# Performance work log

Measured on AMD Instinct MI355X. Metric: run time of the kernel, lower is better.

Reference implementation:

```python
import math
import jax, jax.numpy as jnp
import numpy as np

N = 256  # size (power of 2)
B = 512  # batch
STEEPNESS = 10.0  # cauchy distribution steepness


def _bitonic_network(n):
    # n must be a power of 2; every layer then has exactly n//2 compare-exchanges.
    num_blocks = int(math.log2(n))
    sa_l, sb_l, cmin_l, cmax_l = [], [], [], []
    for block_idx in range(num_blocks):
        for layer_idx in range(block_idx + 1):
            m = 2 ** (block_idx - layer_idx)
            split_a = np.zeros((n // 2, n), np.float32)
            split_b = np.zeros((n // 2, n), np.float32)
            combine_min = np.zeros((n, n // 2), np.float32)
            combine_max = np.zeros((n, n // 2), np.float32)
            count = 0
            for i in range(0, n, 2 * m):
                for j in range(m):
                    ix = i + j
                    a, b = ix, ix + m
                    split_a[count, a] = 1.0
                    split_b[count, b] = 1.0
                    if (ix // 2 ** (block_idx + 1)) % 2 == 1:
                        a, b = b, a
                    combine_min[a, count] = 1.0
                    combine_max[b, count] = 1.0
                    count += 1
            sa_l.append(split_a); sb_l.append(split_b)
            cmin_l.append(combine_min); cmax_l.append(combine_max)
    return (np.stack(sa_l), np.stack(sb_l), np.stack(cmin_l), np.stack(cmax_l))


def setup_inputs() -> dict:
    key = jax.random.key(0)
    vectors = jax.random.normal(key, (B, N), dtype=jnp.float32)
    sa, sb, cmin, cmax = _bitonic_network(N)
    return {
        "vectors": vectors,
        "split_a": jnp.asarray(sa),       # [L, n/2, n]
        "split_b": jnp.asarray(sb),       # [L, n/2, n]
        "combine_min": jnp.asarray(cmin), # [L, n, n/2]
        "combine_max": jnp.asarray(cmax), # [L, n, n/2]
    }


def reference(vectors, split_a, split_b, combine_min, combine_max):
    # Faithful to the given source: x (=vectors) is never updated inside the
    # loop; only the soft permutation matrix X is accumulated and returned.
    Bsz, n = vectors.shape
    X0 = jnp.broadcast_to(jnp.eye(n, dtype=vectors.dtype), (Bsz, n, n))

    def step(X, mats):
        sa, sb, cmin, cmax = mats
        a = vectors @ sa.T  # [B, k]
        b = vectors @ sb.T  # [B, k]
        # cauchy interpolation
        alpha = jnp.arctan(STEEPNESS * (b - a)) / jnp.pi + 0.5  # [B, k]
        aX = jnp.einsum('bij,kj->bik', X, sa)  # [B, n, k]
        bX = jnp.einsum('bij,kj->bik', X, sb)  # [B, n, k]
        al = alpha[:, None, :]
        w_min = al * aX + (1.0 - al) * bX
        w_max = (1.0 - al) * aX + al * bX
        X_new = jnp.einsum('bik,jk->bij', w_max, cmax) + jnp.einsum('bik,jk->bij', w_min, cmin)
        return X_new, None

    X, _ = jax.lax.scan(step, X0, (split_a, split_b, combine_min, combine_max))
    return X
```

## Files before the change

### kernel.cpp

```cpp
#include <hip/hip_runtime.h>
#include <math.h>

typedef float vf4 __attribute__((ext_vector_type(4)));

static constexpr int LLB[36] = {
  0,
  1,0,
  2,1,0,
  3,2,1,0,
  4,3,2,1,0,
  5,4,3,2,1,0,
  6,5,4,3,2,1,0,
  7,6,5,4,3,2,1,0
};
static constexpr int LBLK[36] = {
  0,
  1,1,
  2,2,2,
  3,3,3,3,
  4,4,4,4,4,
  5,5,5,5,5,5,
  6,6,6,6,6,6,6,
  7,7,7,7,7,7,7,7
};

#define BF(ARR, KL, UU) { \
  const int p_ = (((KL) >> lb) << (lb + 1)) | ((KL) & (m - 1)); \
  const int q_ = p_ + m; \
  const float t_  = ARR[p_] - ARR[q_]; \
  const float np_ = fmaf((UU), t_, ARR[q_]); \
  const float nq_ = fmaf(-(UU), t_, ARR[p_]); \
  ARR[p_] = np_; ARR[q_] = nq_; }

__global__ __launch_bounds__(256) void k_gen1(const float* __restrict__ vec,
                                              float* __restrict__ U2,
                                              float4* __restrict__ staged2) {
  const int b = blockIdx.x;
  const int tid = threadIdx.x;
  __shared__ __align__(16) float ub[36 * 128];
  __shared__ float vv[256];
  vv[tid] = vec[b * 256 + tid];
  __syncthreads();

  const int k = tid & 127;
  if (tid < 128) {
    #pragma unroll
    for (int l = 0; l < 18; ++l) {
      const int lb = LLB[l], blk = LBLK[l];
      const int m = 1 << lb;
      const int p = ((k >> lb) << (lb + 1)) | (k & (m - 1));
      const int q = p + m;
      const int d = (p >> (blk + 1)) & 1;
      const float alpha =
          atanf(10.0f * (vv[q] - vv[p])) * 0.3183098861837907f + 0.5f;
      ub[l * 128 + k] = d ? (1.0f - alpha) : alpha;
    }
  } else {
    #pragma unroll
    for (int l = 18; l < 36; ++l) {
      const int lb = LLB[l], blk = LBLK[l];
      const int m = 1 << lb;
      const int p = ((k >> lb) << (lb + 1)) | (k & (m - 1));
      const int q = p + m;
      const int d = (p >> (blk + 1)) & 1;
      const float alpha =
          atanf(10.0f * (vv[q] - vv[p])) * 0.3183098861837907f + 0.5f;
      const float u = d ? (1.0f - alpha) : alpha;
      ub[l * 128 + k] = u;
      if (l >= 21) U2[b * 1920 + (l - 21) * 128 + k] = u;
    }
  }
  __syncthreads();

  const int g  = tid >> 6;
  const int il = tid & 63;
  float r[64];
  #pragma unroll
  for (int j = 0; j < 64; ++j) r[j] = (j == il) ? 1.0f : 0.0f;

  #pragma unroll
  for (int l = 0; l < 21; ++l) {
    const int lb = LLB[l];
    const int m = 1 << lb;
    const float4* ulv = (const float4*)(ub + l * 128 + 32 * g);
    #pragma unroll
    for (int t = 0; t < 8; ++t) {
      const float4 u4 = ulv[t];
      BF(r, 4*t+0, u4.x)
      BF(r, 4*t+1, u4.y)
      BF(r, 4*t+2, u4.z)
      BF(r, 4*t+3, u4.w)
    }
  }

  float4* sp = staged2 + ((size_t)(b * 4 + g) * 16) * 64 + il;
  #pragma unroll
  for (int t = 0; t < 16; ++t)
    sp[t * 64] = make_float4(r[4*t], r[4*t+1], r[4*t+2], r[4*t+3]);
}

__global__ __launch_bounds__(256) void k_phase23(const float* __restrict__ U2,
                                                 const float4* __restrict__ staged2,
                                                 float* __restrict__ out) {
  const int bg = blockIdx.x;
  const int b = bg >> 2;
  const int g = bg & 3;
  const int c  = threadIdx.x >> 6;
  const int rr = threadIdx.x & 63;
  __shared__ float4 ex[2048];
  float y[64];

  const int ub2 = __builtin_amdgcn_readfirstlane(b * 1920);
  const int ap = g >> 1;
  const bool part = ((c >> 1) == ap);
  const int cb = __builtin_amdgcn_readfirstlane(32 * c);

  if (part) {
    const bool sm = ((c & 1) == (g & 1));
    const float* u21 = U2 + ub2 + 64 * ap;
    const float4* sp = staged2 + ((size_t)(b * 4 + g) * 16) * 64 + rr;
    #pragma unroll
    for (int t = 0; t < 16; ++t) {
      const float4 s4 = sp[t * 64];
      const float u0 = u21[4*t+0], u1 = u21[4*t+1];
      const float u2 = u21[4*t+2], u3 = u21[4*t+3];
      y[4*t+0] = s4.x * (sm ? u0 : 1.0f - u0);
      y[4*t+1] = s4.y * (sm ? u1 : 1.0f - u1);
      y[4*t+2] = s4.z * (sm ? u2 : 1.0f - u2);
      y[4*t+3] = s4.w * (sm ? u3 : 1.0f - u3);
    }
    #pragma unroll
    for (int l = 22; l < 28; ++l) {
      const int lb = LLB[l];
      const int m = 1 << lb;
      const float* ul = U2 + ub2 + (l - 21) * 128 + cb;
      #pragma unroll
      for (int kl = 0; kl < 32; ++kl) {
        const float u = ul[kl];
        BF(y, kl, u)
      }
    }
  }

  {
    const float* u28 = U2 + ub2 + 7 * 128 + 64 * (c & 1);
    if (part) {
      #pragma unroll
      for (int t = 0; t < 16; ++t)
        ex[((c & 1) * 16 + t) * 64 + rr] =
            make_float4(y[4*t], y[4*t+1], y[4*t+2], y[4*t+3]);
    }
    __syncthreads();
    if (part) {
      #pragma unroll
      for (int t = 0; t < 16; ++t) {
        y[4*t+0] *= u28[4*t+0];
        y[4*t+1] *= u28[4*t+1];
        y[4*t+2] *= u28[4*t+2];
        y[4*t+3] *= u28[4*t+3];
      }
    } else {
      #pragma unroll
      for (int t = 0; t < 16; ++t) {
        const float4 p4 = ex[((c & 1) * 16 + t) * 64 + rr];
        y[4*t+0] = fmaf(-u28[4*t+0], p4.x, p4.x);
        y[4*t+1] = fmaf(-u28[4*t+1], p4.y, p4.y);
        y[4*t+2] = fmaf(-u28[4*t+2], p4.z, p4.z);
        y[4*t+3] = fmaf(-u28[4*t+3], p4.w, p4.w);
      }
    }
    __syncthreads();
  }

  {
    const float* u29 = U2 + ub2 + 8 * 128 + 64 * (c >> 1);
    const int pc = c ^ 1;
    #pragma unroll
    for (int t = 0; t < 8; ++t)
      ex[(c * 8 + t) * 64 + rr] =
          make_float4(y[4*t], y[4*t+1], y[4*t+2], y[4*t+3]);
    __syncthreads();
    #pragma unroll
    for (int t = 0; t < 8; ++t) {
      const float4 p4 = ex[(pc * 8 + t) * 64 + rr];
      y[4*t+0] = fmaf(u29[4*t+0], y[4*t+0] - p4.x, p4.x);
      y[4*t+1] = fmaf(u29[4*t+1], y[4*t+1] - p4.y, p4.y);
      y[4*t+2] = fmaf(u29[4*t+2], y[4*t+2] - p4.z, p4.z);
      y[4*t+3] = fmaf(u29[4*t+3], y[4*t+3] - p4.w, p4.w);
    }
    __syncthreads();
    #pragma unroll
    for (int t = 8; t < 16; ++t)
      ex[(c * 8 + (t - 8)) * 64 + rr] =
          make_float4(y[4*t], y[4*t+1], y[4*t+2], y[4*t+3]);
    __syncthreads();
    #pragma unroll
    for (int t = 8; t < 16; ++t) {
      const float4 p4 = ex[(pc * 8 + (t - 8)) * 64 + rr];
      y[4*t+0] = fmaf(u29[4*t+0], y[4*t+0] - p4.x, p4.x);
      y[4*t+1] = fmaf(u29[4*t+1], y[4*t+1] - p4.y, p4.y);
      y[4*t+2] = fmaf(u29[4*t+2], y[4*t+2] - p4.z, p4.z);
      y[4*t+3] = fmaf(u29[4*t+3], y[4*t+3] - p4.w, p4.w);
    }
    __syncthreads();
  }

  #pragma unroll
  for (int l = 30; l < 36; ++l) {
    const int lb = LLB[l];
    const int m = 1 << lb;
    const float* ul = U2 + ub2 + (l - 21) * 128 + cb;
    #pragma unroll
    for (int kl = 0; kl < 32; ++kl) {
      const float u = ul[kl];
      BF(y, kl, u)
    }
  }

  float4* out4 = (float4*)out + ((size_t)(b * 256 + g * 64)) * 64;
  const int tid = threadIdx.x;

  if (rr < 32) {
    #pragma unroll
    for (int t = 0; t < 16; ++t)
      ex[rr * 64 + ((c * 16 + t) ^ (rr & 7))] =
          make_float4(y[4*t], y[4*t+1], y[4*t+2], y[4*t+3]);
  }
  __syncthreads();
  #pragma unroll
  for (int it = 0; it < 8; ++it) {
    const int fq = it * 256 + tid;
    const int r_ = fq >> 6;
    const int q_ = fq & 63;
    const float4 v4 = ex[r_ * 64 + (q_ ^ (r_ & 7))];
    __builtin_nontemporal_store(*(const vf4*)&v4, (vf4*)&out4[fq]);
  }
  __syncthreads();
  if (rr >= 32) {
    #pragma unroll
    for (int t = 0; t < 16; ++t)
      ex[(rr - 32) * 64 + ((c * 16 + t) ^ (rr & 7))] =
          make_float4(y[4*t], y[4*t+1], y[4*t+2], y[4*t+3]);
  }
  __syncthreads();
  #pragma unroll
  for (int it = 0; it < 8; ++it) {
    const int fq = it * 256 + tid;
    const int r_ = fq >> 6;
    const int q_ = fq & 63;
    const float4 v4 = ex[r_ * 64 + (q_ ^ (r_ & 7))];
    __builtin_nontemporal_store(*(const vf4*)&v4, (vf4*)&out4[2048 + fq]);
  }
}

extern "C" void kernel_launch(void* const* d_in, const int* in_sizes, int n_in,
                              void* d_out, int out_size, void* d_ws, size_t ws_size,
                              hipStream_t stream) {
  const float* vec = (const float*)d_in[0];
  float* out = (float*)d_out;
  float* U2 = (float*)d_ws;
  float4* staged2 = (float4*)(U2 + (size_t)512 * 1920);

  hipLaunchKernelGGL(k_gen1,    dim3(512),  dim3(256), 0, stream, vec, U2, staged2);
  hipLaunchKernelGGL(k_phase23, dim3(2048), dim3(256), 0, stream, U2, staged2, out);
}
```

Measured before the change: 186.4 us.

## Split rows across lane quads with DPP butterflies and LDS-cached weights

Rewrites the second-phase kernel so each row of the permutation matrix is spread across four lanes. The smallest-stride compare-exchange layers now use DPP lane swaps instead of LDS exchange rounds with block barriers. The per-batch interpolation weights are staged once in shared memory, and the first kernel writes them in a permuted order so that float4 reads line up with the new lane mapping. This is meant to cut LDS round-trips, barriers and global weight loads, at the cost of more complex indexing and a strict dependence on the staging layout matching between the two kernels.

Result: slower. 193.9 us (+4.0%).

```diff
diff --git a/kernel.cpp b/kernel.cpp
--- a/kernel.cpp
+++ b/kernel.cpp
@@ -24,14 +24,6 @@
   7,7,7,7,7,7,7,7
 };
 
-#define BF(ARR, KL, UU) { \
-  const int p_ = (((KL) >> lb) << (lb + 1)) | ((KL) & (m - 1)); \
-  const int q_ = p_ + m; \
-  const float t_  = ARR[p_] - ARR[q_]; \
-  const float np_ = fmaf((UU), t_, ARR[q_]); \
-  const float nq_ = fmaf(-(UU), t_, ARR[p_]); \
-  ARR[p_] = np_; ARR[q_] = nq_; }
-
 __global__ __launch_bounds__(256) void k_gen1(const float* __restrict__ vec,
                                               float* __restrict__ U2,
                                               float4* __restrict__ staged2) {
@@ -66,8 +58,13 @@
       const float alpha =
           atanf(10.0f * (vv[q] - vv[p])) * 0.3183098861837907f + 0.5f;
       const float u = d ? (1.0f - alpha) : alpha;
-      ub[l * 128 + k] = u;
-      if (l >= 21) U2[b * 1920 + (l - 21) * 128 + k] = u;
+      if (l < 21) ub[l * 128 + k] = u;
+      if (l >= 21) {
+        int pos;
+        if (lb >= 2) pos = (k >> 4) * 16 + (k & 3) * 4 + ((k >> 2) & 3);
+        else         pos = (k >> 3) * 8  + (k & 1) * 4 + ((k >> 1) & 3);
+        U2[b * 1920 + (l - 21) * 128 + pos] = u;
+      }
     }
   }
   __syncthreads();
@@ -86,10 +83,18 @@
     #pragma unroll
     for (int t = 0; t < 8; ++t) {
       const float4 u4 = ulv[t];
-      BF(r, 4*t+0, u4.x)
-      BF(r, 4*t+1, u4.y)
-      BF(r, 4*t+2, u4.z)
-      BF(r, 4*t+3, u4.w)
+      #pragma unroll
+      for (int c = 0; c < 4; ++c) {
+        const int kl = 4 * t + c;
+        const int p = ((kl >> lb) << (lb + 1)) | (kl & (m - 1));
+        const int q = p + m;
+        const float u = (c == 0) ? u4.x : (c == 1) ? u4.y : (c == 2) ? u4.z : u4.w;
+        const float t_  = r[p] - r[q];
+        const float np = fmaf(u, t_, r[q]);
+        const float nq = fmaf(-u, t_, r[p]);
+        r[p] = np;
+        r[q] = nq;
+      }
     }
   }
 
@@ -99,157 +104,128 @@
     sp[t * 64] = make_float4(r[4*t], r[4*t+1], r[4*t+2], r[4*t+3]);
 }
 
-__global__ __launch_bounds__(256) void k_phase23(const float* __restrict__ U2,
-                                                 const float4* __restrict__ staged2,
-                                                 float* __restrict__ out) {
+
+#define BFP(KK, LBP, UU) { \
+  const int mp_ = 1 << (LBP); \
+  const int p_ = (((KK) >> (LBP)) << ((LBP) + 1)) | ((KK) & (mp_ - 1)); \
+  const float t_ = y[p_] - y[p_ + mp_]; \
+  const float np_ = fmaf((UU), t_, y[p_ + mp_]); \
+  const float nq_ = fmaf(-(UU), t_, y[p_]); \
+  y[p_] = np_; y[p_ + mp_] = nq_; }
+
+#define INL(LI, LBP, K0, NP) { \
+  const float4* uL4 = (const float4*)(up + (LI) * 128) + t4; \
+  _Pragma("unroll") \
+  for (int kg = (K0) >> 2; kg < ((K0) + (NP)) >> 2; ++kg) { \
+    const float4 u4 = uL4[kg * 4]; \
+    BFP(4*kg+0, LBP, u4.x) BFP(4*kg+1, LBP, u4.y) \
+    BFP(4*kg+2, LBP, u4.z) BFP(4*kg+3, LBP, u4.w) } }
+
+#define DPPBF(AA, XM, UU) { \
+  const float pv_ = __int_as_float(__builtin_amdgcn_mov_dpp( \
+      __float_as_int(y[AA]), (XM), 0xF, 0xF, false)); \
+  y[AA] = fmaf((UU), y[AA] - pv_, pv_); }
+
+#define DPPL(LI, XM, SEL, A0, NA) { \
+  const float4* uD4 = (const float4*)(up + (LI) * 128) + (SEL); \
+  _Pragma("unroll") \
+  for (int ag = (A0) >> 2; ag < ((A0) + (NA)) >> 2; ++ag) { \
+    const float4 u4 = uD4[ag * 2]; \
+    DPPBF(4*ag+0, XM, u4.x) DPPBF(4*ag+1, XM, u4.y) \
+    DPPBF(4*ag+2, XM, u4.z) DPPBF(4*ag+3, XM, u4.w) } }
+
+#define LOADY(BASE) { \
+  _Pragma("unroll") \
+  for (int j = 0; j < 16; ++j) y[(BASE) + j] = sp[j * 256]; }
+
+#define BLK6(RB) { \
+  INL(0, 4, (RB)/2, 16)   \
+  INL(1, 3, (RB)/2, 16)   \
+  INL(2, 2, (RB)/2, 16)   \
+  INL(3, 1, (RB)/2, 16)   \
+  INL(4, 0, (RB)/2, 16)   \
+  DPPL(5, 0x4E, (t4 & 1),  (RB), 32)   \
+  DPPL(6, 0xB1, (t4 >> 1), (RB), 32)   }
+
+__global__ __launch_bounds__(256, 4) void k_phaseC(const float* __restrict__ U2,
+                                                   const float* __restrict__ stagedF,
+                                                   float* __restrict__ out) {
   const int bg = blockIdx.x;
   const int b = bg >> 2;
   const int g = bg & 3;
-  const int c  = threadIdx.x >> 6;
-  const int rr = threadIdx.x & 63;
+  const int tid = threadIdx.x;
+  const int w   = tid >> 6;
+  const int lane = tid & 63;
+  const int t4  = lane & 3;
+  const int r16 = lane >> 2;
+
+  __shared__ __align__(16) float up[1920];
   __shared__ float4 ex[2048];
+
   float y[64];
-
-  const int ub2 = __builtin_amdgcn_readfirstlane(b * 1920);
-  const int ap = g >> 1;
-  const bool part = ((c >> 1) == ap);
-  const int cb = __builtin_amdgcn_readfirstlane(32 * c);
-
-  if (part) {
-    const bool sm = ((c & 1) == (g & 1));
-    const float* u21 = U2 + ub2 + 64 * ap;
-    const float4* sp = staged2 + ((size_t)(b * 4 + g) * 16) * 64 + rr;
-    #pragma unroll
-    for (int t = 0; t < 16; ++t) {
-      const float4 s4 = sp[t * 64];
-      const float u0 = u21[4*t+0], u1 = u21[4*t+1];
-      const float u2 = u21[4*t+2], u3 = u21[4*t+3];
-      y[4*t+0] = s4.x * (sm ? u0 : 1.0f - u0);
-      y[4*t+1] = s4.y * (sm ? u1 : 1.0f - u1);
-      y[4*t+2] = s4.z * (sm ? u2 : 1.0f - u2);
-      y[4*t+3] = s4.w * (sm ? u3 : 1.0f - u3);
-    }
-    #pragma unroll
-    for (int l = 22; l < 28; ++l) {
-      const int lb = LLB[l];
-      const int m = 1 << lb;
-      const float* ul = U2 + ub2 + (l - 21) * 128 + cb;
-      #pragma unroll
-      for (int kl = 0; kl < 32; ++kl) {
-        const float u = ul[kl];
-        BF(y, kl, u)
-      }
-    }
-  }
-
-  {
-    const float* u28 = U2 + ub2 + 7 * 128 + 64 * (c & 1);
-    if (part) {
-      #pragma unroll
-      for (int t = 0; t < 16; ++t)
-        ex[((c & 1) * 16 + t) * 64 + rr] =
-            make_float4(y[4*t], y[4*t+1], y[4*t+2], y[4*t+3]);
-    }
-    __syncthreads();
-    if (part) {
-      #pragma unroll
-      for (int t = 0; t < 16; ++t) {
-        y[4*t+0] *= u28[4*t+0];
-        y[4*t+1] *= u28[4*t+1];
-        y[4*t+2] *= u28[4*t+2];
-        y[4*t+3] *= u28[4*t+3];
-      }
-    } else {
-      #pragma unroll
-      for (int t = 0; t < 16; ++t) {
-        const float4 p4 = ex[((c & 1) * 16 + t) * 64 + rr];
-        y[4*t+0] = fmaf(-u28[4*t+0], p4.x, p4.x);
-        y[4*t+1] = fmaf(-u28[4*t+1], p4.y, p4.y);
-        y[4*t+2] = fmaf(-u28[4*t+2], p4.z, p4.z);
-        y[4*t+3] = fmaf(-u28[4*t+3], p4.w, p4.w);
-      }
-    }
-    __syncthreads();
-  }
-
-  {
-    const float* u29 = U2 + ub2 + 8 * 128 + 64 * (c >> 1);
-    const int pc = c ^ 1;
-    #pragma unroll
-    for (int t = 0; t < 8; ++t)
-      ex[(c * 8 + t) * 64 + rr] =
-          make_float4(y[4*t], y[4*t+1], y[4*t+2], y[4*t+3]);
-    __syncthreads();
-    #pragma unroll
-    for (int t = 0; t < 8; ++t) {
-      const float4 p4 = ex[(pc * 8 + t) * 64 + rr];
-      y[4*t+0] = fmaf(u29[4*t+0], y[4*t+0] - p4.x, p4.x);
-      y[4*t+1] = fmaf(u29[4*t+1], y[4*t+1] - p4.y, p4.y);
-      y[4*t+2] = fmaf(u29[4*t+2], y[4*t+2] - p4.z, p4.z);
-      y[4*t+3] = fmaf(u29[4*t+3], y[4*t+3] - p4.w, p4.w);
-    }
-    __syncthreads();
-    #pragma unroll
-    for (int t = 8; t < 16; ++t)
-      ex[(c * 8 + (t - 8)) * 64 + rr] =
-          make_float4(y[4*t], y[4*t+1], y[4*t+2], y[4*t+3]);
-    __syncthreads();
-    #pragma unroll
-    for (int t = 8; t < 16; ++t) {
-      const float4 p4 = ex[(pc * 8 + (t - 8)) * 64 + rr];
-      y[4*t+0] = fmaf(u29[4*t+0], y[4*t+0] - p4.x, p4.x);
-      y[4*t+1] = fmaf(u29[4*t+1], y[4*t+1] - p4.y, p4.y);
-      y[4*t+2] = fmaf(u29[4*t+2], y[4*t+2] - p4.z, p4.z);
-      y[4*t+3] = fmaf(u29[4*t+3], y[4*t+3] - p4.w, p4.w);
-    }
-    __syncthreads();
-  }
-
-  #pragma unroll
-  for (int l = 30; l < 36; ++l) {
-    const int lb = LLB[l];
-    const int m = 1 << lb;
-    const float* ul = U2 + ub2 + (l - 21) * 128 + cb;
-    #pragma unroll
-    for (int kl = 0; kl < 32; ++kl) {
-      const float u = ul[kl];
-      BF(y, kl, u)
-    }
-  }
-
+  #pragma unroll
+  for (int j = 0; j < 64; ++j) y[j] = 0.0f;
+
+  const float* sp = stagedF + (size_t)bg * 4096 + tid;
+  const float* u2b = U2 + b * 1920;
+  #pragma unroll
+  for (int it = 0; it < 8; ++it) {
+    const int idx = it * 256 + tid;
+    if (idx < 1920) up[idx] = u2b[idx];
+  }
+
+  if (g == 0)      { LOADY(0)  }
+  else if (g == 1) { LOADY(16) }
+  else if (g == 2) { LOADY(32) }
+  else             { LOADY(48) }
+
+  __syncthreads();
+
+  if ((g >> 1) == 0) { BLK6(0) } else { BLK6(32) }
+
+  INL(7,  5, 0, 32)
+  INL(8,  4, 0, 32)
+  INL(9,  3, 0, 32)
+  INL(10, 2, 0, 32)
+  INL(11, 1, 0, 32)
+  INL(12, 0, 0, 32)
+  DPPL(13, 0x4E, (t4 & 1),  0, 64)
+  DPPL(14, 0xB1, (t4 >> 1), 0, 64)
+
+  float* exf = (float*)ex;
   float4* out4 = (float4*)out + ((size_t)(b * 256 + g * 64)) * 64;
-  const int tid = threadIdx.x;
-
-  if (rr < 32) {
-    #pragma unroll
-    for (int t = 0; t < 16; ++t)
-      ex[rr * 64 + ((c * 16 + t) ^ (rr & 7))] =
-          make_float4(y[4*t], y[4*t+1], y[4*t+2], y[4*t+3]);
+
+  if (w < 2) {
+    const int rp = (w << 4) | r16;
+    const int sw = 4 * (r16 & 7);
+    #pragma unroll
+    for (int a = 0; a < 64; ++a)
+      exf[rp * 256 + ((4 * a + t4) ^ sw)] = y[a];
   }
   __syncthreads();
   #pragma unroll
   for (int it = 0; it < 8; ++it) {
     const int fq = it * 256 + tid;
-    const int r_ = fq >> 6;
-    const int q_ = fq & 63;
-    const float4 v4 = ex[r_ * 64 + (q_ ^ (r_ & 7))];
-    __builtin_nontemporal_store(*(const vf4*)&v4, (vf4*)&out4[fq]);
-  }
-  __syncthreads();
-  if (rr >= 32) {
-    #pragma unroll
-    for (int t = 0; t < 16; ++t)
-      ex[(rr - 32) * 64 + ((c * 16 + t) ^ (rr & 7))] =
-          make_float4(y[4*t], y[4*t+1], y[4*t+2], y[4*t+3]);
+    const int rp = fq >> 6, q = fq & 63;
+    const float4 v4 = ex[rp * 64 + (q ^ (rp & 7))];
+    __builtin_nontemporal_store(*(const vf4*)&v4, (vf4*)&out4[rp * 64 + q]);
+  }
+  __syncthreads();
+  if (w >= 2) {
+    const int rp = ((w - 2) << 4) | r16;
+    const int sw = 4 * (r16 & 7);
+    #pragma unroll
+    for (int a = 0; a < 64; ++a)
+      exf[rp * 256 + ((4 * a + t4) ^ sw)] = y[a];
   }
   __syncthreads();
   #pragma unroll
   for (int it = 0; it < 8; ++it) {
     const int fq = it * 256 + tid;
-    const int r_ = fq >> 6;
-    const int q_ = fq & 63;
-    const float4 v4 = ex[r_ * 64 + (q_ ^ (r_ & 7))];
-    __builtin_nontemporal_store(*(const vf4*)&v4, (vf4*)&out4[2048 + fq]);
+    const int rp = fq >> 6, q = fq & 63;
+    const float4 v4 = ex[rp * 64 + (q ^ (rp & 7))];
+    __builtin_nontemporal_store(*(const vf4*)&v4,
+                                (vf4*)&out4[2048 + rp * 64 + q]);
   }
 }
 
@@ -259,8 +235,9 @@
   const float* vec = (const float*)d_in[0];
   float* out = (float*)d_out;
   float* U2 = (float*)d_ws;
-  float4* staged2 = (float4*)(U2 + (size_t)512 * 1920);
-
-  hipLaunchKernelGGL(k_gen1,    dim3(512),  dim3(256), 0, stream, vec, U2, staged2);
-  hipLaunchKernelGGL(k_phase23, dim3(2048), dim3(256), 0, stream, U2, staged2, out);
+  float* staged2 = U2 + (size_t)512 * 1920;
+
+  hipLaunchKernelGGL(k_gen1,   dim3(512),  dim3(256), 0, stream, vec, U2,
+                     (float4*)staged2);
+  hipLaunchKernelGGL(k_phaseC, dim3(2048), dim3(256), 0, stream, U2, staged2, out);
 }
```
